# Kernel tuning notes

Measured on AMD Instinct MI355X. Metric: run time of the kernel, lower is better.

The kernel has to match this reference:

```python
import jax, jax.numpy as jnp
import numpy as np

B, N, G, K = 4, 2048, 8, 16
C_IN = K * 3 + 3  # in_features_size=0 path: conv1 in = 0 + local_n*3 + 3 = 51
CH = [C_IN, 32, 48, 64, 80, 96]  # feature_size(4i, 4i*3) = 16i for i=2..6
THR = 0.1  # weight_threshold


def setup_inputs() -> dict:
    key = jax.random.key(0)
    ks = jax.random.split(key, 3 + 3 * 5)
    inp = {
        "point_cloud": jax.random.normal(ks[0], (B, N, 3), jnp.float32),
        "normals": jax.random.normal(ks[1], (B, N, 3), jnp.float32),
        "dr_w": jax.random.uniform(ks[2], (B, N, G), jnp.float32),
    }
    for i in range(5):
        cin, cout = CH[i], CH[i + 1]
        k0 = 3 + 3 * i
        inp[f"W{i+1}"] = jax.random.normal(ks[k0], (cin, cout), jnp.float32) * (1.0 / np.sqrt(cin))
        inp[f"b{i+1}"] = jnp.zeros((cout,), jnp.float32)
        inp[f"s{i+1}"] = 1.0 + 0.1 * jax.random.normal(ks[k0 + 1], (cout,), jnp.float32)  # BN (eval) scale
        inp[f"o{i+1}"] = 0.01 * jax.random.normal(ks[k0 + 2], (cout,), jnp.float32)      # BN (eval) shift
    return inp


def _forward(point_cloud, normals, dr_w, params):
    # sign-flip group for full (non rotation-only) 3D frames: 8 ops, flips eigenvector columns
    OPS = jnp.array([[1, 1, 1], [1, 1, -1], [1, -1, 1], [1, -1, -1],
                     [-1, 1, 1], [-1, 1, -1], [-1, -1, 1], [-1, -1, -1]], jnp.float32)
    wn = jnp.swapaxes(dr_w, 1, 2)                                  # [B,G,N]
    wsum = dr_w.sum(1)                                             # [B,G]
    wnorm = dr_w / (dr_w.sum(1, keepdims=True) + 1e-6)             # [B,N,G]
    # --- get_frame (weighted): weighted center + weighted covariance + eigh per group ---
    center = jnp.einsum('bnd,bng->bgd', point_cloud, wnorm)        # [B,G,3]
    pc = point_cloud[:, None, :, :] - center[:, :, None, :]        # [B,G,N,3]
    Rm = jnp.einsum('bgnd,bgn,bgne->bgde', pc, wn, pc)             # [B,G,3,3]
    deg = (wsum > 1.0).astype(Rm.dtype)[..., None, None]           # degenerate-group guard
    noise = jax.random.normal(jax.random.key(42), Rm.shape, Rm.dtype)
    lambdas, V = jnp.linalg.eigh(deg * Rm + (1.0 - deg) * noise)
    frames = jax.lax.stop_gradient(V)                              # is_detach_frame=True
    center = jax.lax.stop_gradient(center)
    F_ops = OPS[None, :, None, None, :] * frames[:, None]          # [B,8,G,3,3]
    # --- soft-weighted kNN over points ---
    ww = jnp.einsum('bng,bmg->bnm', dr_w, dr_w)                    # [B,N,N]
    sq = jnp.sum((point_cloud[:, :, None, :] - point_cloud[:, None, :, :]) ** 2, -1)
    d = ww * sq + (1.0 - ww) * 1000.0
    _, idx = jax.lax.top_k(-d, K)                                  # smallest K -> [B,N,K]
    pnts_n = jax.vmap(lambda p, i: p[i])(point_cloud, idx)         # [B,N,K,3]
    # v1 = (1-w)*center + w*pnts_n - center = w*(pnts_n - center)
    v1 = wn[..., None, None] * (pnts_n[:, None] - center[:, :, None, None, :])  # [B,G,N,K,3]
    # v2: weighted normals blended with per-group weighted mean normal
    nw = normals[:, None, :, :] * wn[..., None]                    # [B,G,N,3]
    nmean = nw.sum(2) / (wsum[..., None] + 1e-6)                   # [B,G,3]
    v2 = nw + (1.0 - wn)[..., None] * nmean[:, :, None, :]         # [B,G,N,3]
    # apply equivariant frames: (F_ops^T @ v^T)^T == v @ F_ops
    f1 = jnp.einsum('bgnkd,bogde->bognke', v1, F_ops)              # [B,8,G,N,K,3]
    f2 = jnp.einsum('bgnd,bogde->bogne', v2, F_ops)                # [B,8,G,N,3]
    x = jnp.concatenate([f1.reshape(B, 8, G, N, K * 3), f2], -1)   # [B,8,G,N,51]
    # MinkowskiLinear + BN(eval affine) + ReLU stack, applied densely then masked
    for (W, b, s, o) in params:
        x = jax.nn.relu((x @ W + b) * s + o)
    mask = (wn >= THR).astype(x.dtype)[:, None, :, :, None]        # weight_threshold filter
    return x * mask                                                # [B,8,G,N,96]


def reference(point_cloud, normals, dr_w,
              W1, b1, s1, o1, W2, b2, s2, o2, W3, b3, s3, o3,
              W4, b4, s4, o4, W5, b5, s5, o5):
    params = [(W1, b1, s1, o1), (W2, b2, s2, o2), (W3, b3, s3, o3),
              (W4, b4, s4, o4), (W5, b5, s5, o5)]
    return _forward(point_cloud, normals, dr_w, params)
```

## Files before the change

kernel.cpp:

```cpp
#include <hip/hip_runtime.h>
#include <math.h>

#define NPTS 2048
#define BATCH 4
#define NG 8
#define KNN_K 16
#define FR_OFF 512
#define IDX_OFF 1024
#define WOFF_F (IDX_OFF + BATCH * NPTS * KNN_K)
#define FLOATMAX 3.402823466e38f

typedef __attribute__((ext_vector_type(8))) short bf16x8;
typedef __attribute__((ext_vector_type(4))) float f32x4;

__device__ inline unsigned short bf16_rne(float x) {
  unsigned u = __float_as_uint(x);
  u += 0x7FFFu + ((u >> 16) & 1u);
  return (unsigned short)(u >> 16);
}
__device__ inline float bf16_f(unsigned short h) {
  return __uint_as_float(((unsigned)h) << 16);
}

__device__ inline unsigned pack_hl(float h) {
  unsigned u = __float_as_uint(h);
  float rem = h - __uint_as_float(u & 0xffff0000u);
  unsigned v = __float_as_uint(rem);
  v += 0x7fffu + ((v >> 16) & 1u);
  return __builtin_amdgcn_perm(u, v, 0x07060302u);
}

__device__ inline void unpack8(const unsigned* __restrict__ p, bf16x8& ah, bf16x8& al) {
  union U { unsigned u[4]; bf16x8 v; };
  uint4 x = *(const uint4*)p;
  uint4 y = *(const uint4*)(p + 4);
  U a, b;
  a.u[0] = __builtin_amdgcn_perm(x.y, x.x, 0x07060302u);
  a.u[1] = __builtin_amdgcn_perm(x.w, x.z, 0x07060302u);
  a.u[2] = __builtin_amdgcn_perm(y.y, y.x, 0x07060302u);
  a.u[3] = __builtin_amdgcn_perm(y.w, y.z, 0x07060302u);
  b.u[0] = __builtin_amdgcn_perm(x.y, x.x, 0x05040100u);
  b.u[1] = __builtin_amdgcn_perm(x.w, x.z, 0x05040100u);
  b.u[2] = __builtin_amdgcn_perm(y.y, y.x, 0x05040100u);
  b.u[3] = __builtin_amdgcn_perm(y.w, y.z, 0x05040100u);
  ah = a.v;
  al = b.v;
}

__device__ inline float slapy2f(float x, float y) {
  float ax = fabsf(x), ay = fabsf(y);
  float w = fmaxf(ax, ay), z = fminf(ax, ay);
  if (z == 0.f) return w;
  float q = z / w;
  return w * sqrtf(1.f + q * q);
}

__device__ inline void slartgf(float f, float g, float& c, float& s, float& r) {
  if (g == 0.f) { c = 1.f; s = 0.f; r = f; }
  else if (f == 0.f) { c = 0.f; s = (g >= 0.f) ? 1.f : -1.f; r = fabsf(g); }
  else {
    float d = sqrtf(f * f + g * g);
    c = fabsf(f) / d;
    r = (f >= 0.f) ? d : -d;
    s = g / r;
  }
}

__device__ void slaev2f(float a, float b, float c, float& rt1, float& rt2, float& cs1, float& sn1) {
  float sm = a + c, df = a - c, adf = fabsf(df), tb = b + b, ab = fabsf(tb);
  float acmx, acmn;
  if (fabsf(a) > fabsf(c)) { acmx = a; acmn = c; } else { acmx = c; acmn = a; }
  float rt;
  if (adf > ab) { float t = ab / adf; rt = adf * sqrtf(1.f + t * t); }
  else if (adf < ab) { float t = adf / ab; rt = ab * sqrtf(1.f + t * t); }
  else rt = ab * sqrtf(2.f);
  int sgn1;
  if (sm < 0.f) { rt1 = 0.5f * (sm - rt); sgn1 = -1; rt2 = (acmx / rt1) * acmn - (b / rt1) * b; }
  else if (sm > 0.f) { rt1 = 0.5f * (sm + rt); sgn1 = 1; rt2 = (acmx / rt1) * acmn - (b / rt1) * b; }
  else { rt1 = 0.5f * rt; rt2 = -0.5f * rt; sgn1 = 1; }
  float cs; int sgn2;
  if (df >= 0.f) { cs = df + rt; sgn2 = 1; } else { cs = df - rt; sgn2 = -1; }
  float acs = fabsf(cs);
  if (acs > ab) {
    float ct = -tb / cs;
    sn1 = 1.f / sqrtf(1.f + ct * ct);
    cs1 = ct * sn1;
  } else {
    if (ab == 0.f) { cs1 = 1.f; sn1 = 0.f; }
    else {
      float tn = -cs / tb;
      cs1 = 1.f / sqrtf(1.f + tn * tn);
      sn1 = tn * cs1;
    }
  }
  if (sgn1 == sgn2) { float tn = cs1; cs1 = -sn1; sn1 = tn; }
}

__device__ void steqr3(float d[3], float e[2], float Z[3][3]) {
  const float eps = 5.9604645e-08f;
  const float eps2 = eps * eps;
  const float safmin = 1.17549435e-38f;
  const int nmaxit = 90;
  const int n = 3;
  int jtot = 0;
  int l1 = 0;
  while (l1 <= n - 1) {
    if (l1 > 0) e[l1 - 1] = 0.f;
    int m;
    for (m = l1; m <= n - 2; m++) {
      float tst = fabsf(e[m]);
      if (tst == 0.f) break;
      if (tst <= (sqrtf(fabsf(d[m])) * sqrtf(fabsf(d[m + 1]))) * eps) { e[m] = 0.f; break; }
    }
    int l = l1, lend = m;
    l1 = m + 1;
    if (lend == l) continue;
    if (fabsf(d[lend]) < fabsf(d[l])) { int tmp = l; l = lend; lend = tmp; }
    if (lend > l) {
      for (;;) {
        int mm = lend;
        if (l != lend) {
          for (mm = l; mm <= lend - 1; mm++) {
            float tst = e[mm] * e[mm];
            if (tst <= eps2 * fabsf(d[mm]) * fabsf(d[mm + 1]) + safmin) break;
          }
        }
        if (mm < lend) e[mm] = 0.f;
        float p = d[l];
        if (mm == l) {
          d[l] = p; l++;
          if (l <= lend) continue; else break;
        }
        if (mm == l + 1) {
          float rt1, rt2, c, s;
          slaev2f(d[l], e[l], d[l + 1], rt1, rt2, c, s);
          #pragma unroll
          for (int i = 0; i < 3; i++) {
            float tp = Z[i][l + 1];
            Z[i][l + 1] = c * tp - s * Z[i][l];
            Z[i][l] = s * tp + c * Z[i][l];
          }
          d[l] = rt1; d[l + 1] = rt2; e[l] = 0.f;
          l += 2;
          if (l <= lend) continue; else break;
        }
        if (jtot == nmaxit) break;
        jtot++;
        float g = (d[l + 1] - p) / (2.f * e[l]);
        float r = slapy2f(g, 1.f);
        g = d[mm] - p + e[l] / (g + copysignf(r, g));
        float s = 1.f, c = 1.f;
        p = 0.f;
        float cs[2], sn[2];
        for (int i = mm - 1; i >= l; i--) {
          float f = s * e[i];
          float bb = c * e[i];
          slartgf(g, f, c, s, r);
          if (i != mm - 1) e[i + 1] = r;
          g = d[i + 1] - p;
          r = (d[i] - g) * s + 2.f * c * bb;
          p = s * r;
          d[i + 1] = g + p;
          g = c * r - bb;
          cs[i] = c; sn[i] = -s;
        }
        for (int jj = mm - l - 1; jj >= 0; jj--) {
          float c_ = cs[l + jj], s_ = sn[l + jj];
          #pragma unroll
          for (int i = 0; i < 3; i++) {
            float tp = Z[i][l + jj + 1];
            Z[i][l + jj + 1] = c_ * tp - s_ * Z[i][l + jj];
            Z[i][l + jj] = s_ * tp + c_ * Z[i][l + jj];
          }
        }
        d[l] -= p;
        e[l] = g;
      }
    } else {
      for (;;) {
        int mm = lend;
        if (l != lend) {
          for (mm = l; mm >= lend + 1; mm--) {
            float tst = e[mm - 1] * e[mm - 1];
            if (tst <= eps2 * fabsf(d[mm]) * fabsf(d[mm - 1]) + safmin) break;
          }
        }
        if (mm > lend) e[mm - 1] = 0.f;
        float p = d[l];
        if (mm == l) {
          d[l] = p; l--;
          if (l >= lend) continue; else break;
        }
        if (mm == l - 1) {
          float rt1, rt2, c, s;
          slaev2f(d[l - 1], e[l - 1], d[l], rt1, rt2, c, s);
          #pragma unroll
          for (int i = 0; i < 3; i++) {
            float tp = Z[i][l];
            Z[i][l] = c * tp - s * Z[i][l - 1];
            Z[i][l - 1] = s * tp + c * Z[i][l - 1];
          }
          d[l - 1] = rt1; d[l] = rt2; e[l - 1] = 0.f;
          l -= 2;
          if (l >= lend) continue; else break;
        }
        if (jtot == nmaxit) break;
        jtot++;
        float g = (d[l - 1] - p) / (2.f * e[l - 1]);
        float r = slapy2f(g, 1.f);
        g = d[mm] - p + e[l - 1] / (g + copysignf(r, g));
        float s = 1.f, c = 1.f;
        p = 0.f;
        float cs[2], sn[2];
        for (int i = mm; i <= l - 1; i++) {
          float f = s * e[i];
          float bb = c * e[i];
          slartgf(g, f, c, s, r);
          if (i != mm) e[i - 1] = r;
          g = d[i] - p;
          r = (d[i + 1] - g) * s + 2.f * c * bb;
          p = s * r;
          d[i] = g + p;
          g = c * r - bb;
          cs[i] = c; sn[i] = s;
        }
        for (int jj = 0; jj <= l - mm - 1; jj++) {
          float c_ = cs[mm + jj], s_ = sn[mm + jj];
          #pragma unroll
          for (int i = 0; i < 3; i++) {
            float tp = Z[i][mm + jj + 1];
            Z[i][mm + jj + 1] = c_ * tp - s_ * Z[i][mm + jj];
            Z[i][mm + jj] = s_ * tp + c_ * Z[i][mm + jj];
          }
        }
        d[l] -= p;
        e[l - 1] = g;
      }
    }
  }
  for (int ii = 1; ii < 3; ii++) {
    int i = ii - 1, k = i;
    float p = d[i];
    for (int j = ii; j < 3; j++) if (d[j] < p) { k = j; p = d[j]; }
    if (k != i) {
      d[k] = d[i]; d[i] = p;
      for (int r2 = 0; r2 < 3; r2++) {
        float tp = Z[r2][i]; Z[r2][i] = Z[r2][k]; Z[r2][k] = tp;
      }
    }
  }
}

__device__ void eigh_one(float* __restrict__ ws, int id) {
  const float* st = ws + id * 16;
  float A00 = st[7], A10 = st[8], A11 = st[9], A20 = st[10], A21 = st[11], A22 = st[12];

  float d[3], e[2];
  float tau = 0.f, u2 = 0.f;
  d[0] = A00;
  float alpha = A10, x31 = A20;
  if (x31 == 0.f) {
    tau = 0.f; u2 = 0.f;
    d[1] = A11; d[2] = A22; e[0] = alpha; e[1] = A21;
  } else {
    float nrm = slapy2f(alpha, fabsf(x31));
    float beta = (alpha >= 0.f) ? -nrm : nrm;
    tau = (beta - alpha) / beta;
    u2 = (1.f / (alpha - beta)) * x31;
    float x1 = tau * (A11 + A21 * u2);
    float x2 = tau * (A21 + A22 * u2);
    float al = -0.5f * tau * (x1 + x2 * u2);
    x1 = x1 + al;
    x2 = x2 + al * u2;
    d[1] = A11 - 2.f * x1;
    e[1] = A21 - (u2 * x1 + x2);
    d[2] = A22 - 2.f * (u2 * x2);
    e[0] = beta;
  }

  float Z[3][3] = {{1.f, 0.f, 0.f}, {0.f, 1.f, 0.f}, {0.f, 0.f, 1.f}};
  steqr3(d, e, Z);

  if (tau != 0.f) {
    for (int j = 0; j < 3; j++) {
      float w = Z[1][j] + u2 * Z[2][j];
      float tw = tau * w;
      Z[1][j] -= tw;
      Z[2][j] -= tw * u2;
    }
  }
  float* fr = ws + FR_OFF + id * 9;
  for (int dd = 0; dd < 3; dd++)
    for (int ee = 0; ee < 3; ee++)
      fr[dd * 3 + ee] = Z[dd][ee];
}

__global__ void prep_kernel(const float* __restrict__ pc, const float* __restrict__ nrm,
                            const float* __restrict__ drw,
                            const float* __restrict__ W1, const float* __restrict__ W2,
                            const float* __restrict__ W3, const float* __restrict__ W4,
                            const float* __restrict__ W5, float* __restrict__ ws) {
  __shared__ float red[256];
  int t = threadIdx.x;

  if (blockIdx.x < 32) {
    int bg = blockIdx.x;
    int b = bg >> 3, g = bg & 7;

    float sw = 0.f, sp0 = 0.f, sp1 = 0.f, sp2 = 0.f, sn0 = 0.f, sn1 = 0.f, sn2 = 0.f;
    for (int n = t; n < NPTS; n += 256) {
      float w = drw[((size_t)b * NPTS + n) * NG + g];
      const float* p = pc + ((size_t)b * NPTS + n) * 3;
      const float* nr = nrm + ((size_t)b * NPTS + n) * 3;
      sw += w;
      sp0 += w * p[0]; sp1 += w * p[1]; sp2 += w * p[2];
      sn0 += w * nr[0]; sn1 += w * nr[1]; sn2 += w * nr[2];
    }

    auto blockReduce = [&](float v) -> float {
      red[t] = v; __syncthreads();
      for (int s = 128; s > 0; s >>= 1) {
        if (t < s) red[t] += red[t + s];
        __syncthreads();
      }
      float r = red[0];
      __syncthreads();
      return r;
    };

    float Sw = blockReduce(sw);
    float inv = 1.f / (Sw + 1e-6f);
    float C0 = blockReduce(sp0) * inv;
    float C1 = blockReduce(sp1) * inv;
    float C2 = blockReduce(sp2) * inv;
    float M0 = blockReduce(sn0) * inv;
    float M1 = blockReduce(sn1) * inv;
    float M2 = blockReduce(sn2) * inv;

    float r00 = 0.f, r10 = 0.f, r11 = 0.f, r20 = 0.f, r21 = 0.f, r22 = 0.f;
    for (int n = t; n < NPTS; n += 256) {
      float w = drw[((size_t)b * NPTS + n) * NG + g];
      const float* p = pc + ((size_t)b * NPTS + n) * 3;
      float p0 = p[0] - C0, p1 = p[1] - C1, p2 = p[2] - C2;
      r00 += w * p0 * p0;
      r10 += w * p1 * p0;
      r11 += w * p1 * p1;
      r20 += w * p2 * p0;
      r21 += w * p2 * p1;
      r22 += w * p2 * p2;
    }
    float R00 = blockReduce(r00);
    float R10 = blockReduce(r10);
    float R11 = blockReduce(r11);
    float R20 = blockReduce(r20);
    float R21 = blockReduce(r21);
    float R22 = blockReduce(r22);

    if (t == 0) {
      float* st = ws + bg * 16;
      st[0] = Sw;
      st[1] = C0; st[2] = C1; st[3] = C2;
      st[4] = M0; st[5] = M1; st[6] = M2;
      st[7] = R00; st[8] = R10; st[9] = R11; st[10] = R20; st[11] = R21; st[12] = R22;
    }
    return;
  }

  if (t >= 64) return;
  const int FBt[5] = {0, 4, 7, 15, 25};
  const int NTs[5] = {2, 3, 4, 5, 6};
  const int CINs[5] = {51, 32, 48, 64, 80};
  const int COUTs[5] = {32, 48, 64, 80, 96};
  const float* Ws[5] = {W1, W2, W3, W4, W5};

  int fp = blockIdx.x - 32;
  int layer = 0;
  while (layer < 4 && fp >= FBt[layer + 1]) layer++;
  int rel = fp - FBt[layer];
  int kt = rel / NTs[layer], nt = rel % NTs[layer];
  int lane = t;
  int c = nt * 16 + (lane & 15);
  int q = lane >> 4;
  int cin = CINs[layer], cout = COUTs[layer];
  const float* W = Ws[layer];

  unsigned short* wb = (unsigned short*)(ws + WOFF_F);
  unsigned short* dH = wb + fp * 1024 + lane * 8;
  unsigned short* dL = dH + 512;
  for (int i = 0; i < 8; i++) {
    int k = kt * 32 + q * 8 + i;
    float w = (k < cin) ? W[(size_t)k * cout + c] : 0.f;
    unsigned short hb = bf16_rne(w);
    dH[i] = hb;
    dL[i] = bf16_rne(w - bf16_f(hb));
  }
}

__global__ __launch_bounds__(256, 4) void knn_eigh_kernel(const float* __restrict__ pc,
                                                          const float* __restrict__ drw,
                                                          int* __restrict__ idxout,
                                                          float* __restrict__ ws) {
  if (blockIdx.x < 32) {
    if (threadIdx.x == 0) eigh_one(ws, blockIdx.x);
    return;
  }
  int t = threadIdx.x;
  int lane = t & 63;
  int q = (blockIdx.x - 32) * 4 + (t >> 6);
  int b = q >> 11;
  int n = q & (NPTS - 1);

  const float* qp = pc + ((size_t)b * NPTS + n) * 3;
  float q0 = qp[0], q1 = qp[1], q2 = qp[2];
  const float4* qw4 = (const float4*)(drw + ((size_t)b * NPTS + n) * NG);
  float4 qa = qw4[0], qb = qw4[1];

  float d[32];
  #pragma unroll
  for (int j = 0; j < 32; j++) {
    int m = j * 64 + lane;
    const float4* mw4 = (const float4*)(drw + ((size_t)b * NPTS + m) * NG);
    float4 ma = mw4[0], mb = mw4[1];
    float ww = qa.x * ma.x + qa.y * ma.y + qa.z * ma.z + qa.w * ma.w
             + qb.x * mb.x + qb.y * mb.y + qb.z * mb.z + qb.w * mb.w;
    const float* mp = pc + ((size_t)b * NPTS + m) * 3;
    float dx = q0 - mp[0], dy = q1 - mp[1], dz = q2 - mp[2];
    float sq = dx * dx + dy * dy + dz * dz;
    d[j] = ww * sq + (1.f - ww) * 1000.f;
    if ((j & 3) == 3) __builtin_amdgcn_sched_barrier(0);
  }

  int myres = 0;
  #pragma unroll 1
  for (int r = 0; r < KNN_K; r++) {
    float bd = d[0];
    int bj = 0;
    #pragma unroll
    for (int j = 1; j < 32; j++) {
      if (d[j] < bd) { bd = d[j]; bj = j; }
    }
    int gm = bj * 64 + lane;
    #pragma unroll
    for (int s = 1; s < 64; s <<= 1) {
      float od = __shfl_xor(bd, s, 64);
      int om = __shfl_xor(gm, s, 64);
      if (od < bd || (od == bd && om < gm)) { bd = od; gm = om; }
    }
    if (lane == r) myres = gm;
    int ls = gm & 63, js = gm >> 6;
    if (lane == ls) {
      #pragma unroll
      for (int j = 0; j < 32; j++) {
        if (j == js) d[j] = FLOATMAX;
      }
    }
  }
  if (lane < KNN_K) idxout[(size_t)q * KNN_K + lane] = myres;
}

#define PST0 84
#define PST1 68

template <int CIN, int COUT, int FB, int SIN, int SOUT>
__device__ inline void mfma_layerP(const unsigned short* __restrict__ wfr,
                                   const unsigned* inP, unsigned* outP,
                                   const float* __restrict__ Bb, const float* __restrict__ Ss,
                                   const float* __restrict__ Oo, int lane, int wv) {
  constexpr int KT = (CIN + 31) / 32;
  constexpr int NT = COUT / 16;
  int r = lane & 15, q = lane >> 4;
  int arow = (wv * 16 + r) * SIN;

  f32x4 acc[NT];
  #pragma unroll
  for (int i = 0; i < NT; i++) acc[i] = (f32x4){0.f, 0.f, 0.f, 0.f};

  #pragma unroll
  for (int kt = 0; kt < KT; kt++) {
    bf16x8 ah, al;
    unpack8(inP + arow + kt * 32 + q * 8, ah, al);
    #pragma unroll
    for (int nt = 0; nt < NT; nt++) {
      int fid = FB + kt * NT + nt;
      bf16x8 bh = *(const bf16x8*)(wfr + fid * 1024 + lane * 8);
      bf16x8 bl = *(const bf16x8*)(wfr + fid * 1024 + 512 + lane * 8);
      acc[nt] = __builtin_amdgcn_mfma_f32_16x16x32_bf16(ah, bh, acc[nt], 0, 0, 0);
      acc[nt] = __builtin_amdgcn_mfma_f32_16x16x32_bf16(ah, bl, acc[nt], 0, 0, 0);
      acc[nt] = __builtin_amdgcn_mfma_f32_16x16x32_bf16(al, bh, acc[nt], 0, 0, 0);
    }
  }

  #pragma unroll
  for (int nt = 0; nt < NT; nt++) {
    int c = nt * 16 + r;
    float bb = Bb[c], ss = Ss[c], oo = Oo[c];
    #pragma unroll
    for (int j = 0; j < 4; j++) {
      float h = fmaxf(fmaf(acc[nt][j] + bb, ss, oo), 0.f);
      outP[(wv * 16 + q * 4 + j) * SOUT + c] = pack_hl(h);
    }
  }
}

__global__ __launch_bounds__(256, 4) void mlp_kernel(
    const float* __restrict__ pc, const float* __restrict__ nrm, const float* __restrict__ drw,
    const int* __restrict__ kidx, const float* __restrict__ ws,
    const float* __restrict__ B1, const float* __restrict__ S1, const float* __restrict__ O1,
    const float* __restrict__ B2, const float* __restrict__ S2, const float* __restrict__ O2,
    const float* __restrict__ B3, const float* __restrict__ S3, const float* __restrict__ O3,
    const float* __restrict__ B4, const float* __restrict__ S4, const float* __restrict__ O4,
    const float* __restrict__ B5, const float* __restrict__ S5, const float* __restrict__ O5,
    float* __restrict__ out) {
  __shared__ __align__(16) unsigned smem[9728];
  unsigned* PK0 = smem;
  unsigned* PK1 = smem + 5376;

  int t = threadIdx.x;
  int bi = blockIdx.x;
  int b = bi >> 11;
  int g = (bi >> 8) & 7;
  int n0 = (bi & 255) << 3;
  int bg = b * 8 + g;

  for (int z = t; z < 1088; z += 256) {
    int row = z / 17;
    int cc = z - row * 17;
    int col = (cc < 13) ? (51 + cc) : (67 + cc);
    PK0[row * PST0 + col] = 0u;
  }
  if (t < 12) PK1[t] = 0u;

  if (t < 128) {
    int i = t >> 4, kk = t & 15;
    int n = n0 + i;
    int id = kidx[((size_t)b * NPTS + n) * KNN_K + kk];
    const float* p = pc + ((size_t)b * NPTS + id) * 3;
    const float* fr = ws + FR_OFF + bg * 9;
    const float* ct = ws + bg * 16 + 1;
    float w = drw[((size_t)b * NPTS + n) * NG + g];
    float v0 = w * (p[0] - ct[0]);
    float v1 = w * (p[1] - ct[1]);
    float v2 = w * (p[2] - ct[2]);
    #pragma unroll
    for (int e = 0; e < 3; e++) {
      float gv = v0 * fr[e] + v1 * fr[3 + e] + v2 * fr[6 + e];
      unsigned pk = pack_hl(gv);
      int f = 3 * kk + e;
      #pragma unroll
      for (int op = 0; op < 8; op++) {
        int sb = (e == 0) ? (op >> 2) : (e == 1) ? (op >> 1) : op;
        unsigned pv = (sb & 1) ? (pk ^ 0x80008000u) : pk;
        PK0[(i * 8 + op) * PST0 + f] = pv;
      }
    }
  } else if (t < 136) {
    int i = t - 128;
    int n = n0 + i;
    float w = drw[((size_t)b * NPTS + n) * NG + g];
    const float* nr = nrm + ((size_t)b * NPTS + n) * 3;
    const float* fr = ws + FR_OFF + bg * 9;
    const float* nm = ws + bg * 16 + 4;
    float v0 = nr[0] * w + (1.f - w) * nm[0];
    float v1 = nr[1] * w + (1.f - w) * nm[1];
    float v2 = nr[2] * w + (1.f - w) * nm[2];
    #pragma unroll
    for (int e = 0; e < 3; e++) {
      float gv = v0 * fr[e] + v1 * fr[3 + e] + v2 * fr[6 + e];
      unsigned pk = pack_hl(gv);
      int f = 48 + e;
      #pragma unroll
      for (int op = 0; op < 8; op++) {
        int sb = (e == 0) ? (op >> 2) : (e == 1) ? (op >> 1) : op;
        unsigned pv = (sb & 1) ? (pk ^ 0x80008000u) : pk;
        PK0[(i * 8 + op) * PST0 + f] = pv;
      }
    }
  }
  __syncthreads();

  const unsigned short* wfr = (const unsigned short*)(ws + WOFF_F);
  int lane = t & 63;
  int wv = t >> 6;

  mfma_layerP<51, 32, 0, PST0, PST1>(wfr, PK0, PK1, B1, S1, O1, lane, wv);
  mfma_layerP<32, 48, 4, PST1, PST0>(wfr, PK1, PK0, B2, S2, O2, lane, wv);
  mfma_layerP<48, 64, 7, PST0, PST1>(wfr, PK0, PK1, B3, S3, O3, lane, wv);
  mfma_layerP<64, 80, 15, PST1, PST0>(wfr, PK1, PK0, B4, S4, O4, lane, wv);

  {
    constexpr int KT = 3, NT = 6, FB = 25;
    int r = lane & 15, q = lane >> 4;
    int arow = (wv * 16 + r) * PST0;
    f32x4 acc[NT];
    #pragma unroll
    for (int i = 0; i < NT; i++) acc[i] = (f32x4){0.f, 0.f, 0.f, 0.f};
    #pragma unroll
    for (int kt = 0; kt < KT; kt++) {
      bf16x8 ah, al;
      unpack8(PK0 + arow + kt * 32 + q * 8, ah, al);
      #pragma unroll
      for (int nt = 0; nt < NT; nt++) {
        int fid = FB + kt * NT + nt;
        bf16x8 bh = *(const bf16x8*)(wfr + fid * 1024 + lane * 8);
        bf16x8 bl = *(const bf16x8*)(wfr + fid * 1024 + 512 + lane * 8);
        acc[nt] = __builtin_amdgcn_mfma_f32_16x16x32_bf16(ah, bh, acc[nt], 0, 0, 0);
        acc[nt] = __builtin_amdgcn_mfma_f32_16x16x32_bf16(ah, bl, acc[nt], 0, 0, 0);
        acc[nt] = __builtin_amdgcn_mfma_f32_16x16x32_bf16(al, bh, acc[nt], 0, 0, 0);
      }
    }
    int i = 2 * wv + (q >> 1);
    int n = n0 + i;
    float wlane = drw[((size_t)b * NPTS + n) * NG + g];
    float maskv = (wlane >= 0.1f) ? 1.f : 0.f;
    int opbase = (q & 1) * 4;
    #pragma unroll
    for (int nt = 0; nt < NT; nt++) {
      int c = nt * 16 + r;
      float bb = B5[c], ss = S5[c], oo = O5[c];
      #pragma unroll
      for (int j = 0; j < 4; j++) {
        int op = opbase + j;
        float h = fmaxf(fmaf(acc[nt][j] + bb, ss, oo), 0.f);
        out[((((size_t)(b * 8 + op)) * NG + g) * NPTS + n) * 96 + c] = h * maskv;
      }
    }
  }
}

extern "C" void kernel_launch(void* const* d_in, const int* in_sizes, int n_in,
                              void* d_out, int out_size, void* d_ws, size_t ws_size,
                              hipStream_t stream) {
  const float* pc = (const float*)d_in[0];
  const float* nrm = (const float*)d_in[1];
  const float* drw = (const float*)d_in[2];
  const float* W1 = (const float*)d_in[3];
  const float* B1 = (const float*)d_in[4];
  const float* S1 = (const float*)d_in[5];
  const float* O1 = (const float*)d_in[6];
  const float* W2 = (const float*)d_in[7];
  const float* B2 = (const float*)d_in[8];
  const float* S2 = (const float*)d_in[9];
  const float* O2 = (const float*)d_in[10];
  const float* W3 = (const float*)d_in[11];
  const float* B3 = (const float*)d_in[12];
  const float* S3 = (const float*)d_in[13];
  const float* O3 = (const float*)d_in[14];
  const float* W4 = (const float*)d_in[15];
  const float* B4 = (const float*)d_in[16];
  const float* S4 = (const float*)d_in[17];
  const float* O4 = (const float*)d_in[18];
  const float* W5 = (const float*)d_in[19];
  const float* B5 = (const float*)d_in[20];
  const float* S5 = (const float*)d_in[21];
  const float* O5 = (const float*)d_in[22];
  float* out = (float*)d_out;
  float* wsf = (float*)d_ws;
  int* idxw = (int*)(wsf + IDX_OFF);

  prep_kernel<<<75, 256, 0, stream>>>(pc, nrm, drw, W1, W2, W3, W4, W5, wsf);
  knn_eigh_kernel<<<32 + BATCH * NPTS / 4, 256, 0, stream>>>(pc, drw, idxw, wsf);
  mlp_kernel<<<BATCH * NG * (NPTS / 8), 256, 0, stream>>>(
      pc, nrm, drw, idxw, wsf,
      B1, S1, O1, B2, S2, O2, B3, S3, O3,
      B4, S4, O4, B5, S5, O5, out);
}
```

Measured before the change: 388.2 us.

## Merge prep and kNN/eigh kernels and fold BN scale into weights

The prep and kNN launches become one front kernel. The eigen-decomposition now runs right after the covariance reduction, and the kNN blocks follow the weight-packing blocks in the same grid. The batch-norm scale is folded into the packed bf16 weights, and bias*scale+shift is precomputed into one bias vector. This cuts the MLP epilogue to an add and ReLU and removes one launch and its boundary. Explicit s_barrier calls are added between MLP layers, which may add synchronisation. Folding the scale before bf16 splitting slightly changes rounding.

```diff
diff --git a/kernel.cpp b/kernel.cpp
--- a/kernel.cpp
+++ b/kernel.cpp
@@ -8,6 +8,7 @@
 #define FR_OFF 512
 #define IDX_OFF 1024
 #define WOFF_F (IDX_OFF + BATCH * NPTS * KNN_K)
+#define WOFF_B (WOFF_F + 22016)
 #define FLOATMAX 3.402823466e38f
 
 typedef __attribute__((ext_vector_type(8))) short bf16x8;
@@ -251,10 +252,8 @@
   }
 }
 
-__device__ void eigh_one(float* __restrict__ ws, int id) {
-  const float* st = ws + id * 16;
-  float A00 = st[7], A10 = st[8], A11 = st[9], A20 = st[10], A21 = st[11], A22 = st[12];
-
+__device__ void eigh_compute(float A00, float A10, float A11, float A20, float A21,
+                             float A22, float* __restrict__ fr) {
   float d[3], e[2];
   float tau = 0.f, u2 = 0.f;
   d[0] = A00;
@@ -289,17 +288,23 @@
       Z[2][j] -= tw * u2;
     }
   }
-  float* fr = ws + FR_OFF + id * 9;
   for (int dd = 0; dd < 3; dd++)
     for (int ee = 0; ee < 3; ee++)
       fr[dd * 3 + ee] = Z[dd][ee];
 }
 
-__global__ void prep_kernel(const float* __restrict__ pc, const float* __restrict__ nrm,
-                            const float* __restrict__ drw,
-                            const float* __restrict__ W1, const float* __restrict__ W2,
-                            const float* __restrict__ W3, const float* __restrict__ W4,
-                            const float* __restrict__ W5, float* __restrict__ ws) {
+__global__ __launch_bounds__(256, 4) void front_kernel(
+    const float* __restrict__ pc, const float* __restrict__ nrm,
+    const float* __restrict__ drw,
+    const float* __restrict__ W1, const float* __restrict__ W2,
+    const float* __restrict__ W3, const float* __restrict__ W4,
+    const float* __restrict__ W5,
+    const float* __restrict__ B1, const float* __restrict__ S1, const float* __restrict__ O1,
+    const float* __restrict__ B2, const float* __restrict__ S2, const float* __restrict__ O2,
+    const float* __restrict__ B3, const float* __restrict__ S3, const float* __restrict__ O3,
+    const float* __restrict__ B4, const float* __restrict__ S4, const float* __restrict__ O4,
+    const float* __restrict__ B5, const float* __restrict__ S5, const float* __restrict__ O5,
+    int* __restrict__ idxout, float* __restrict__ ws) {
   __shared__ float red[256];
   int t = threadIdx.x;
 
@@ -358,55 +363,61 @@
 
     if (t == 0) {
       float* st = ws + bg * 16;
-      st[0] = Sw;
       st[1] = C0; st[2] = C1; st[3] = C2;
       st[4] = M0; st[5] = M1; st[6] = M2;
-      st[7] = R00; st[8] = R10; st[9] = R11; st[10] = R20; st[11] = R21; st[12] = R22;
+      eigh_compute(R00, R10, R11, R20, R21, R22, ws + FR_OFF + bg * 9);
     }
     return;
   }
 
-  if (t >= 64) return;
-  const int FBt[5] = {0, 4, 7, 15, 25};
-  const int NTs[5] = {2, 3, 4, 5, 6};
-  const int CINs[5] = {51, 32, 48, 64, 80};
-  const int COUTs[5] = {32, 48, 64, 80, 96};
-  const float* Ws[5] = {W1, W2, W3, W4, W5};
-
-  int fp = blockIdx.x - 32;
-  int layer = 0;
-  while (layer < 4 && fp >= FBt[layer + 1]) layer++;
-  int rel = fp - FBt[layer];
-  int kt = rel / NTs[layer], nt = rel % NTs[layer];
-  int lane = t;
-  int c = nt * 16 + (lane & 15);
-  int q = lane >> 4;
-  int cin = CINs[layer], cout = COUTs[layer];
-  const float* W = Ws[layer];
-
-  unsigned short* wb = (unsigned short*)(ws + WOFF_F);
-  unsigned short* dH = wb + fp * 1024 + lane * 8;
-  unsigned short* dL = dH + 512;
-  for (int i = 0; i < 8; i++) {
-    int k = kt * 32 + q * 8 + i;
-    float w = (k < cin) ? W[(size_t)k * cout + c] : 0.f;
-    unsigned short hb = bf16_rne(w);
-    dH[i] = hb;
-    dL[i] = bf16_rne(w - bf16_f(hb));
-  }
-}
-
-__global__ __launch_bounds__(256, 4) void knn_eigh_kernel(const float* __restrict__ pc,
-                                                          const float* __restrict__ drw,
-                                                          int* __restrict__ idxout,
-                                                          float* __restrict__ ws) {
-  if (blockIdx.x < 32) {
-    if (threadIdx.x == 0) eigh_one(ws, blockIdx.x);
+  if (blockIdx.x < 75) {
+    if (t >= 64) return;
+    const int FBt[5] = {0, 4, 7, 15, 25};
+    const int NTs[5] = {2, 3, 4, 5, 6};
+    const int CINs[5] = {51, 32, 48, 64, 80};
+    const int COUTs[5] = {32, 48, 64, 80, 96};
+    const float* Ws[5] = {W1, W2, W3, W4, W5};
+    const float* Ss[5] = {S1, S2, S3, S4, S5};
+
+    int fp = blockIdx.x - 32;
+    int layer = 0;
+    while (layer < 4 && fp >= FBt[layer + 1]) layer++;
+    int rel = fp - FBt[layer];
+    int kt = rel / NTs[layer], nt = rel % NTs[layer];
+    int lane = t;
+    int c = nt * 16 + (lane & 15);
+    int q = lane >> 4;
+    int cin = CINs[layer], cout = COUTs[layer];
+    const float* W = Ws[layer];
+    float sc = Ss[layer][c];
+
+    unsigned short* wb = (unsigned short*)(ws + WOFF_F);
+    unsigned short* dH = wb + fp * 1024 + lane * 8;
+    unsigned short* dL = dH + 512;
+    for (int i = 0; i < 8; i++) {
+      int k = kt * 32 + q * 8 + i;
+      float w = (k < cin) ? W[(size_t)k * cout + c] * sc : 0.f;
+      unsigned short hb = bf16_rne(w);
+      dH[i] = hb;
+      dL[i] = bf16_rne(w - bf16_f(hb));
+    }
+
+    if (fp == 0) {
+      const int CUM[5] = {0, 32, 80, 144, 224};
+      const float* Bs[5] = {B1, B2, B3, B4, B5};
+      const float* Os[5] = {O1, O2, O3, O4, O5};
+      for (int idx = t; idx < 320; idx += 64) {
+        int ly = 4;
+        while (ly > 0 && idx < CUM[ly]) ly--;
+        int cc = idx - CUM[ly];
+        ws[WOFF_B + idx] = fmaf(Bs[ly][cc], Ss[ly][cc], Os[ly][cc]);
+      }
+    }
     return;
   }
-  int t = threadIdx.x;
+
   int lane = t & 63;
-  int q = (blockIdx.x - 32) * 4 + (t >> 6);
+  int q = (blockIdx.x - 75) * 4 + (t >> 6);
   int b = q >> 11;
   int n = q & (NPTS - 1);
 
@@ -464,8 +475,7 @@
 template <int CIN, int COUT, int FB, int SIN, int SOUT>
 __device__ inline void mfma_layerP(const unsigned short* __restrict__ wfr,
                                    const unsigned* inP, unsigned* outP,
-                                   const float* __restrict__ Bb, const float* __restrict__ Ss,
-                                   const float* __restrict__ Oo, int lane, int wv) {
+                                   const float* __restrict__ bias, int lane, int wv) {
   constexpr int KT = (CIN + 31) / 32;
   constexpr int NT = COUT / 16;
   int r = lane & 15, q = lane >> 4;
@@ -493,10 +503,10 @@
   #pragma unroll
   for (int nt = 0; nt < NT; nt++) {
     int c = nt * 16 + r;
-    float bb = Bb[c], ss = Ss[c], oo = Oo[c];
+    float bb = bias[c];
     #pragma unroll
     for (int j = 0; j < 4; j++) {
-      float h = fmaxf(fmaf(acc[nt][j] + bb, ss, oo), 0.f);
+      float h = fmaxf(acc[nt][j] + bb, 0.f);
       outP[(wv * 16 + q * 4 + j) * SOUT + c] = pack_hl(h);
     }
   }
@@ -505,11 +515,6 @@
 __global__ __launch_bounds__(256, 4) void mlp_kernel(
     const float* __restrict__ pc, const float* __restrict__ nrm, const float* __restrict__ drw,
     const int* __restrict__ kidx, const float* __restrict__ ws,
-    const float* __restrict__ B1, const float* __restrict__ S1, const float* __restrict__ O1,
-    const float* __restrict__ B2, const float* __restrict__ S2, const float* __restrict__ O2,
-    const float* __restrict__ B3, const float* __restrict__ S3, const float* __restrict__ O3,
-    const float* __restrict__ B4, const float* __restrict__ S4, const float* __restrict__ O4,
-    const float* __restrict__ B5, const float* __restrict__ S5, const float* __restrict__ O5,
     float* __restrict__ out) {
   __shared__ __align__(16) unsigned smem[9728];
   unsigned* PK0 = smem;
@@ -579,13 +584,18 @@
   __syncthreads();
 
   const unsigned short* wfr = (const unsigned short*)(ws + WOFF_F);
+  const float* bias = ws + WOFF_B;
   int lane = t & 63;
   int wv = t >> 6;
 
-  mfma_layerP<51, 32, 0, PST0, PST1>(wfr, PK0, PK1, B1, S1, O1, lane, wv);
-  mfma_layerP<32, 48, 4, PST1, PST0>(wfr, PK1, PK0, B2, S2, O2, lane, wv);
-  mfma_layerP<48, 64, 7, PST0, PST1>(wfr, PK0, PK1, B3, S3, O3, lane, wv);
-  mfma_layerP<64, 80, 15, PST1, PST0>(wfr, PK1, PK0, B4, S4, O4, lane, wv);
+  mfma_layerP<51, 32, 0, PST0, PST1>(wfr, PK0, PK1, bias + 0, lane, wv);
+  __builtin_amdgcn_s_barrier();
+  mfma_layerP<32, 48, 4, PST1, PST0>(wfr, PK1, PK0, bias + 32, lane, wv);
+  __builtin_amdgcn_s_barrier();
+  mfma_layerP<48, 64, 7, PST0, PST1>(wfr, PK0, PK1, bias + 80, lane, wv);
+  __builtin_amdgcn_s_barrier();
+  mfma_layerP<64, 80, 15, PST1, PST0>(wfr, PK1, PK0, bias + 144, lane, wv);
+  __builtin_amdgcn_s_barrier();
 
   {
     constexpr int KT = 3, NT = 6, FB = 25;
@@ -613,14 +623,15 @@
     float wlane = drw[((size_t)b * NPTS + n) * NG + g];
     float maskv = (wlane >= 0.1f) ? 1.f : 0.f;
     int opbase = (q & 1) * 4;
+    const float* b5 = ws + WOFF_B + 224;
     #pragma unroll
     for (int nt = 0; nt < NT; nt++) {
       int c = nt * 16 + r;
-      float bb = B5[c], ss = S5[c], oo = O5[c];
+      float bb = b5[c];
       #pragma unroll
       for (int j = 0; j < 4; j++) {
         int op = opbase + j;
-        float h = fmaxf(fmaf(acc[nt][j] + bb, ss, oo), 0.f);
+        float h = fmaxf(acc[nt][j] + bb, 0.f);
         out[((((size_t)(b * 8 + op)) * NG + g) * NPTS + n) * 96 + c] = h * maskv;
       }
     }
@@ -657,10 +668,10 @@
   float* wsf = (float*)d_ws;
   int* idxw = (int*)(wsf + IDX_OFF);
 
-  prep_kernel<<<75, 256, 0, stream>>>(pc, nrm, drw, W1, W2, W3, W4, W5, wsf);
-  knn_eigh_kernel<<<32 + BATCH * NPTS / 4, 256, 0, stream>>>(pc, drw, idxw, wsf);
+  front_kernel<<<75 + BATCH * NPTS / 4, 256, 0, stream>>>(
+      pc, nrm, drw, W1, W2, W3, W4, W5,
+      B1, S1, O1, B2, S2, O2, B3, S3, O3, B4, S4, O4, B5, S5, O5,
+      idxw, wsf);
   mlp_kernel<<<BATCH * NG * (NPTS / 8), 256, 0, stream>>>(
-      pc, nrm, drw, idxw, wsf,
-      B1, S1, O1, B2, S2, O2, B3, S3, O3,
-      B4, S4, O4, B5, S5, O5, out);
-}
+      pc, nrm, drw, idxw, wsf, out);
+}
```

New measurement: 370.6 us. 1.05x faster.
